# Performance work log

Hardware: AMD Instinct MI355X
Metric: run time of the kernel (lower is better)

Reference implementation:

```python
import jax, jax.numpy as jnp
import numpy as np

B, T, D = 4, 2048, 1024
H, KD, VD = 16, 64, 64  # num_heads, key_dim, value_dim; H*KD == D


def setup_inputs() -> dict:
    key = jax.random.key(0)
    ks = jax.random.split(key, 10)
    s = 0.02
    return {
        "q_in": jax.random.normal(ks[0], (B, T, D), jnp.float32),
        "v_in": jax.random.normal(ks[1], (B, T, D), jnp.float32),
        "Wq": jax.random.normal(ks[2], (D, H * KD), jnp.float32) * s,
        "bq": jnp.zeros((H * KD,), jnp.float32),
        "Wk": jax.random.normal(ks[3], (D, H * KD), jnp.float32) * s,
        "bk": jnp.zeros((H * KD,), jnp.float32),
        "Wv": jax.random.normal(ks[4], (D, H * VD), jnp.float32) * s,
        "bv": jnp.zeros((H * VD,), jnp.float32),
        "Wo": jax.random.normal(ks[5], (H * VD, D), jnp.float32) * s,
        "bo": jnp.zeros((D,), jnp.float32),
    }


def reference(q_in, v_in, Wq, bq, Wk, bk, Wv, bv, Wo, bo):
    # QKV projections (key defaults to value input)
    q = q_in @ Wq + bq                      # [B,T,H*KD]
    k = v_in @ Wk + bk                      # [B,T,H*KD]
    v = v_in @ Wv + bv                      # [B,T,H*VD]
    q = q.reshape(B, T, H, KD)
    k = k.reshape(B, T, H, KD)
    v = v.reshape(B, T, H, VD)
    # scaled dot-product attention, scores materialized as [B,H,Tq,Tv]
    q = q / jnp.sqrt(jnp.asarray(KD, q.dtype))
    scores = jnp.einsum('bqnh,bvnh->bnqv', q, k)
    weights = jax.nn.softmax(scores, axis=-1)
    out = jnp.einsum('bnqv,bvnh->bqnh', weights, v)  # [B,Tq,H,VD]
    out = out.reshape(B, T, H * VD)
    return out @ Wo + bo                    # [B,T,D]
```

## Files before the change

### kernel.cpp

```cpp
#include <hip/hip_runtime.h>

#define BATCH  4
#define T_SEQ  2048
#define NH     16
#define DMODEL 1024
#define HD     64

typedef float    f32x4 __attribute__((ext_vector_type(4)));
typedef _Float16 f16x8 __attribute__((ext_vector_type(8)));
typedef _Float16 f16x4 __attribute__((ext_vector_type(4)));
typedef __fp16   h16x2 __attribute__((ext_vector_type(2)));

#define LOG2E 1.44269504088896f

__device__ __forceinline__ void lds_load16(const void* g, void* l) {
  __builtin_amdgcn_global_load_lds((const __attribute__((address_space(1))) void*)g,
                                   (__attribute__((address_space(3))) void*)l, 16, 0, 0);
}

__device__ __forceinline__ f16x4 pack4_f16(float a, float b, float c, float d) {
  union { h16x2 h[2]; f16x4 f; } u;
  u.h[0] = __builtin_amdgcn_cvt_pkrtz(a, b);
  u.h[1] = __builtin_amdgcn_cvt_pkrtz(c, d);
  return u.f;
}

__global__ __launch_bounds__(256) void cast2_f32_to_f16(
    const float* __restrict__ a, const float* __restrict__ bsrc,
    _Float16* __restrict__ oa, _Float16* __restrict__ ob, int n4) {
  const float* in = blockIdx.y ? bsrc : a;
  _Float16* out = blockIdx.y ? ob : oa;
  int i = blockIdx.x * 256 + threadIdx.x;
  if (i < n4) {
    float4 v = ((const float4*)in)[i];
    f16x4 o = { (_Float16)v.x, (_Float16)v.y, (_Float16)v.z, (_Float16)v.w };
    ((f16x4*)out)[i] = o;
  }
}

__global__ __launch_bounds__(256) void transcast_w4(
    const float* __restrict__ W0, const float* __restrict__ W1,
    const float* __restrict__ W2, const float* __restrict__ W3,
    _Float16* __restrict__ T0, _Float16* __restrict__ T1,
    _Float16* __restrict__ T2, _Float16* __restrict__ T3) {
  const float* W; _Float16* Wt;
  switch (blockIdx.z) {
    case 0: W = W0; Wt = T0; break;
    case 1: W = W1; Wt = T1; break;
    case 2: W = W2; Wt = T2; break;
    default: W = W3; Wt = T3; break;
  }
  __shared__ float L[64][65];
  const int n0 = blockIdx.x * 64, k0 = blockIdx.y * 64;
  const int tx = threadIdx.x & 15, ty = threadIdx.x >> 4;
#pragma unroll
  for (int i = 0; i < 4; ++i) {
    float4 v = *(const float4*)&W[(size_t)(k0 + ty + 16 * i) * DMODEL + n0 + tx * 4];
    L[ty + 16 * i][tx * 4 + 0] = v.x;
    L[ty + 16 * i][tx * 4 + 1] = v.y;
    L[ty + 16 * i][tx * 4 + 2] = v.z;
    L[ty + 16 * i][tx * 4 + 3] = v.w;
  }
  __syncthreads();
#pragma unroll
  for (int i = 0; i < 4; ++i) {
    int n = n0 + ty + 16 * i;
    f16x4 o;
#pragma unroll
    for (int j = 0; j < 4; ++j) o[j] = (_Float16)L[tx * 4 + j][ty + 16 * i];
    *(f16x4*)&Wt[(size_t)n * DMODEL + k0 + tx * 4] = o;
  }
}

__device__ __forceinline__ void gemm_big_body(
    const _Float16* __restrict__ A, const _Float16* __restrict__ Wt,
    const float* __restrict__ bias, void* __restrict__ Cout, float scale,
    int mode, _Float16* As, _Float16* Bs) {
  const int K = DMODEL;
  const int lane = threadIdx.x & 63, wave = threadIdx.x >> 6;
  const int bid = blockIdx.x + blockIdx.y * gridDim.x;
  const int m0 = ((bid & 7) * 4 + ((bid >> 3) & 3)) * 256;
  const int n0 = (bid >> 5) * 128;
  const int wm = (wave & 1) * 8;
  const int wn = (wave >> 1) * 4;
  const int m16 = lane & 15, quad = lane >> 4;

  const _Float16* ap[8]; const _Float16* bp[4];
#pragma unroll
  for (int j = 0; j < 8; ++j) {
    int g = wave * 8 + j;
    ap[j] = A + (size_t)(m0 + (g >> 1) * 16 + m16) * K + (g & 1) * 32 + quad * 8;
  }
#pragma unroll
  for (int j = 0; j < 4; ++j) {
    int g = wave * 4 + j;
    bp[j] = Wt + (size_t)(n0 + (g >> 1) * 16 + m16) * K + (g & 1) * 32 + quad * 8;
  }

  f32x4 acc[8][4] = {};

  for (int k0 = 0; k0 < 1024; k0 += 64) {
    __syncthreads();
#pragma unroll
    for (int j = 0; j < 8; ++j) lds_load16(ap[j] + k0, As + (wave * 8 + j) * 512);
#pragma unroll
    for (int j = 0; j < 4; ++j) lds_load16(bp[j] + k0, Bs + (wave * 4 + j) * 512);
    __syncthreads();
#pragma unroll
    for (int s = 0; s < 2; ++s) {
      f16x8 bf[4];
#pragma unroll
      for (int t = 0; t < 4; ++t)
        bf[t] = *(const f16x8*)(Bs + (((wn + t) * 2 + s) * 64 + lane) * 8);
#pragma unroll
      for (int mi = 0; mi < 8; ++mi) {
        f16x8 af = *(const f16x8*)(As + (((wm + mi) * 2 + s) * 64 + lane) * 8);
#pragma unroll
        for (int ni = 0; ni < 4; ++ni)
          acc[mi][ni] = __builtin_amdgcn_mfma_f32_16x16x32_f16(af, bf[ni], acc[mi][ni], 0, 0, 0);
      }
    }
  }

  if (mode == 2) {
#pragma unroll
    for (int mi = 0; mi < 8; ++mi)
#pragma unroll
      for (int ni = 0; ni < 4; ++ni) {
        int row = m0 + (wm + mi) * 16 + quad * 4;
        int col = n0 + (wn + ni) * 16 + m16;
        int bb = row >> 11, tt = row & (T_SEQ - 1);
        int hh = col >> 6, dd = col & 63;
        float bv = bias[col];
        f16x4 pv = pack4_f16(acc[mi][ni][0] + bv, acc[mi][ni][1] + bv,
                             acc[mi][ni][2] + bv, acc[mi][ni][3] + bv);
        *(f16x4*)&((_Float16*)Cout)[(((size_t)bb * NH + hh) * HD + dd) * T_SEQ + tt] = pv;
      }
  } else {
#pragma unroll
    for (int mi = 0; mi < 8; ++mi)
#pragma unroll
      for (int r = 0; r < 4; ++r) {
        int row = m0 + (wm + mi) * 16 + quad * 4 + r;
#pragma unroll
        for (int ni = 0; ni < 4; ++ni) {
          int col = n0 + (wn + ni) * 16 + m16;
          float v = (acc[mi][ni][r] + bias[col]) * scale;
          ((_Float16*)Cout)[(size_t)row * DMODEL + col] = (_Float16)v;
        }
      }
  }
}

__global__ __launch_bounds__(256, 2) void gemm_qkv(
    const _Float16* __restrict__ Aq, const _Float16* __restrict__ Av,
    const _Float16* __restrict__ Wq, const _Float16* __restrict__ Wk,
    const _Float16* __restrict__ Wv,
    const float* __restrict__ bq, const float* __restrict__ bk,
    const float* __restrict__ bv,
    _Float16* __restrict__ Cq, _Float16* __restrict__ Ck, _Float16* __restrict__ Cv) {
  __shared__ _Float16 As[256 * 64];
  __shared__ _Float16 Bs[128 * 64];
  const _Float16* A; const _Float16* Wt; const float* bias; _Float16* C;
  float scale; int mode;
  if (blockIdx.z == 0)      { A = Aq; Wt = Wq; bias = bq; C = Cq; scale = 0.125f * LOG2E; mode = 0; }
  else if (blockIdx.z == 1) { A = Av; Wt = Wk; bias = bk; C = Ck; scale = 1.f; mode = 0; }
  else                      { A = Av; Wt = Wv; bias = bv; C = Cv; scale = 1.f; mode = 2; }
  gemm_big_body(A, Wt, bias, C, scale, mode, As, Bs);
}

__global__ __launch_bounds__(256, 3) void gemm_out(
    const _Float16* __restrict__ A, const _Float16* __restrict__ Wt,
    const float* __restrict__ bias, float* __restrict__ Cout) {
  __shared__ _Float16 As[128 * 64], Bs[128 * 64];
  const int K = DMODEL;
  const int lane = threadIdx.x & 63, wave = threadIdx.x >> 6;
  const int bid = blockIdx.x + blockIdx.y * gridDim.x;
  const int m0 = ((bid & 7) * 8 + ((bid >> 3) & 7)) * 128;
  const int n0 = (bid >> 6) * 128;
  const int wm = (wave & 1) * 4, wn = (wave >> 1) * 4;
  const int m16 = lane & 15, quad = lane >> 4;

  const _Float16* ap[4]; const _Float16* bp[4];
#pragma unroll
  for (int i = 0; i < 4; ++i) {
    int gi = wave * 4 + i;
    int row = (gi >> 1) * 16 + m16;
    int kof = (gi & 1) * 32 + quad * 8;
    ap[i] = A  + (size_t)(m0 + row) * K + kof;
    bp[i] = Wt + (size_t)(n0 + row) * K + kof;
  }

  f32x4 acc[4][4] = {};

  for (int k0 = 0; k0 < 1024; k0 += 64) {
    __syncthreads();
#pragma unroll
    for (int i = 0; i < 4; ++i) {
      lds_load16(ap[i] + k0, As + (wave * 4 + i) * 512);
      lds_load16(bp[i] + k0, Bs + (wave * 4 + i) * 512);
    }
    __syncthreads();
#pragma unroll
    for (int s = 0; s < 2; ++s) {
      f16x8 af[4], bf[4];
#pragma unroll
      for (int t = 0; t < 4; ++t) {
        af[t] = *(const f16x8*)(As + (((wm + t) * 2 + s) * 64 + lane) * 8);
        bf[t] = *(const f16x8*)(Bs + (((wn + t) * 2 + s) * 64 + lane) * 8);
      }
#pragma unroll
      for (int mi = 0; mi < 4; ++mi)
#pragma unroll
        for (int ni = 0; ni < 4; ++ni)
          acc[mi][ni] = __builtin_amdgcn_mfma_f32_16x16x32_f16(af[mi], bf[ni], acc[mi][ni], 0, 0, 0);
    }
  }

#pragma unroll
  for (int mi = 0; mi < 4; ++mi)
#pragma unroll
    for (int r = 0; r < 4; ++r) {
      int row = m0 + (wm + mi) * 16 + quad * 4 + r;
#pragma unroll
      for (int ni = 0; ni < 4; ++ni) {
        int col = n0 + (wn + ni) * 16 + m16;
        Cout[(size_t)row * DMODEL + col] = acc[mi][ni][r] + bias[col];
      }
    }
}

__global__ __launch_bounds__(256, 2) void attn_mfma(
    const _Float16* __restrict__ Q, const _Float16* __restrict__ Kb,
    const _Float16* __restrict__ Vt, _Float16* __restrict__ O) {
  __shared__ _Float16 Ks[64 * 64], Vs[64 * 64];
  __shared__ _Float16 Ps[4 * 4096];

  const int lane = threadIdx.x & 63, wave = threadIdx.x >> 6;
  const int m16 = lane & 15, quad = lane >> 4;
  const int h = blockIdx.x;
  const int q0 = blockIdx.y * 256;
  const int b = blockIdx.z;
  const int wq = wave * 64;
  const int wbase = wave * 4096;

  f16x8 qf[4][2];
#pragma unroll
  for (int mi = 0; mi < 4; ++mi)
#pragma unroll
    for (int ki = 0; ki < 2; ++ki) {
      int q = q0 + wq + mi * 16 + m16;
      qf[mi][ki] = *(const f16x8*)(Q + (((size_t)b * T_SEQ + q) * NH + h) * HD + ki * 32 + quad * 8);
    }

  const _Float16 *kp[2], *vp[2];
#pragma unroll
  for (int i = 0; i < 2; ++i) {
    int g = wave * 128 + i * 64 + lane;
    int tk = (g >> 7) * 16 + (g & 15);
    int dkof = ((g >> 6) & 1) * 32 + ((g >> 4) & 3) * 8;
    kp[i] = Kb + (((size_t)b * T_SEQ + tk) * NH + h) * HD + dkof;
    int dvof = (g >> 7) * 16 + (g & 15);
    int tv = ((g >> 6) & 1) * 32 + ((g >> 4) & 3) * 8;
    vp[i] = Vt + (((size_t)b * NH + h) * HD + dvof) * T_SEQ + tv;
  }

  int pw[4][4];
#pragma unroll
  for (int mi = 0; mi < 4; ++mi)
#pragma unroll
    for (int nt = 0; nt < 4; ++nt) {
      int kt = nt >> 1;
      int q8 = ((nt & 1) << 1) | (quad >> 1);
      pw[mi][nt] = wbase + ((mi * 2 + kt) * 64 + q8 * 16 + m16) * 8 + (quad & 1) * 4;
    }

  const f16x8 onef = {(_Float16)1, (_Float16)1, (_Float16)1, (_Float16)1,
                      (_Float16)1, (_Float16)1, (_Float16)1, (_Float16)1};

  f32x4 o_acc[4][4] = {};
  f32x4 l_acc[4] = {};

  for (int kv = 0; kv < T_SEQ; kv += 64) {
    __syncthreads();
#pragma unroll
    for (int i = 0; i < 2; ++i) {
      lds_load16(kp[i] + (size_t)kv * (NH * HD), Ks + (wave * 2 + i) * 512);
      lds_load16(vp[i] + kv, Vs + (wave * 2 + i) * 512);
    }
    __syncthreads();

    f32x4 st[4][4] = {};
#pragma unroll
    for (int nt = 0; nt < 4; ++nt)
#pragma unroll
      for (int ki = 0; ki < 2; ++ki) {
        f16x8 kf = *(const f16x8*)(Ks + ((nt * 2 + ki) * 64 + lane) * 8);
#pragma unroll
        for (int mi = 0; mi < 4; ++mi)
          st[mi][nt] = __builtin_amdgcn_mfma_f32_16x16x32_f16(kf, qf[mi][ki], st[mi][nt], 0, 0, 0);
      }

#pragma unroll
    for (int mi = 0; mi < 4; ++mi)
#pragma unroll
      for (int nt = 0; nt < 4; ++nt) {
        f16x4 p = pack4_f16(__builtin_amdgcn_exp2f(st[mi][nt][0]),
                            __builtin_amdgcn_exp2f(st[mi][nt][1]),
                            __builtin_amdgcn_exp2f(st[mi][nt][2]),
                            __builtin_amdgcn_exp2f(st[mi][nt][3]));
        *(f16x4*)(Ps + pw[mi][nt]) = p;
      }

#pragma unroll
    for (int kt = 0; kt < 2; ++kt) {
      f16x8 pf[4];
#pragma unroll
      for (int mi = 0; mi < 4; ++mi) {
        pf[mi] = *(const f16x8*)(Ps + wbase + ((mi * 2 + kt) * 64 + lane) * 8);
        l_acc[mi] = __builtin_amdgcn_mfma_f32_16x16x32_f16(pf[mi], onef, l_acc[mi], 0, 0, 0);
      }
#pragma unroll
      for (int nd = 0; nd < 4; ++nd) {
        f16x8 vf = *(const f16x8*)(Vs + ((nd * 2 + kt) * 64 + lane) * 8);
#pragma unroll
        for (int mi = 0; mi < 4; ++mi)
          o_acc[mi][nd] = __builtin_amdgcn_mfma_f32_16x16x32_f16(pf[mi], vf, o_acc[mi][nd], 0, 0, 0);
      }
    }
  }

#pragma unroll
  for (int mi = 0; mi < 4; ++mi)
#pragma unroll
    for (int r = 0; r < 4; ++r) {
      float inv = 1.f / l_acc[mi][r];
      int q = q0 + wq + mi * 16 + quad * 4 + r;
#pragma unroll
      for (int nd = 0; nd < 4; ++nd) {
        int d = nd * 16 + m16;
        O[(((size_t)b * T_SEQ + q) * NH + h) * HD + d] = (_Float16)(o_acc[mi][nd][r] * inv);
      }
    }
}

extern "C" void kernel_launch(void* const* d_in, const int* in_sizes, int n_in,
                              void* d_out, int out_size, void* d_ws, size_t ws_size,
                              hipStream_t stream) {
  const float* q_in = (const float*)d_in[0];
  const float* v_in = (const float*)d_in[1];
  const float* Wq   = (const float*)d_in[2];
  const float* bq   = (const float*)d_in[3];
  const float* Wk   = (const float*)d_in[4];
  const float* bk   = (const float*)d_in[5];
  const float* Wv   = (const float*)d_in[6];
  const float* bv   = (const float*)d_in[7];
  const float* Wo   = (const float*)d_in[8];
  const float* bo   = (const float*)d_in[9];
  float* out = (float*)d_out;

  const size_t MB = 1u << 20;
  char* ws = (char*)d_ws;
  _Float16* q16  = (_Float16*)(ws);
  _Float16* v16  = (_Float16*)(ws + 16 * MB);
  _Float16* qbuf = (_Float16*)(ws + 32 * MB);
  _Float16* kbuf = (_Float16*)(ws + 48 * MB);
  _Float16* vtb  = (_Float16*)(ws + 64 * MB);
  _Float16* Wqt  = (_Float16*)(ws + 80 * MB);
  _Float16* Wkt  = (_Float16*)(ws + 82 * MB);
  _Float16* Wvt  = (_Float16*)(ws + 84 * MB);
  _Float16* Wot  = (_Float16*)(ws + 86 * MB);

  const int n4 = BATCH * T_SEQ * DMODEL / 4;
  cast2_f32_to_f16<<<dim3(n4 / 256, 2), 256, 0, stream>>>(q_in, v_in, q16, v16, n4);

  transcast_w4<<<dim3(16, 16, 4), 256, 0, stream>>>(Wq, Wk, Wv, Wo, Wqt, Wkt, Wvt, Wot);

  gemm_qkv<<<dim3(8, 32, 3), 256, 0, stream>>>(q16, v16, Wqt, Wkt, Wvt, bq, bk, bv,
                                               qbuf, kbuf, vtb);

  attn_mfma<<<dim3(16, 8, 4), 256, 0, stream>>>(qbuf, kbuf, vtb, qbuf);

  gemm_out<<<dim3(8, 64), 256, 0, stream>>>(qbuf, Wot, bo, out);
}
```

Baseline: 333.6 us.

## Double-buffer LDS in projection GEMMs with 512-thread blocks and shared body

Rewrites the QKV and output projection GEMMs to use double-buffered LDS tiles. The next K-tile is prefetched while MFMAs run on the current one, which leaves one barrier per iteration. Blocks grow to 8 waves, each owning a 64x64 sub-tile, and the output GEMM now uses the same 256x128 tile body as QKV (grid halved). Costs are doubled LDS use (96KB per block), which may limit occupancy, and fewer blocks for the output GEMM.

Result: slower. 345.8 us (+3.6%).

```diff
diff --git a/kernel.cpp b/kernel.cpp
--- a/kernel.cpp
+++ b/kernel.cpp
@@ -72,63 +72,75 @@
   }
 }
 
-__device__ __forceinline__ void gemm_big_body(
+__device__ __forceinline__ void gemm2_body(
     const _Float16* __restrict__ A, const _Float16* __restrict__ Wt,
     const float* __restrict__ bias, void* __restrict__ Cout, float scale,
-    int mode, _Float16* As, _Float16* Bs) {
+    int mode, _Float16* As0, _Float16* As1, _Float16* Bs0, _Float16* Bs1) {
   const int K = DMODEL;
   const int lane = threadIdx.x & 63, wave = threadIdx.x >> 6;
   const int bid = blockIdx.x + blockIdx.y * gridDim.x;
   const int m0 = ((bid & 7) * 4 + ((bid >> 3) & 3)) * 256;
   const int n0 = (bid >> 5) * 128;
-  const int wm = (wave & 1) * 8;
-  const int wn = (wave >> 1) * 4;
+  const int wm4 = (wave & 3) * 4;
+  const int wn4 = (wave >> 2) * 4;
   const int m16 = lane & 15, quad = lane >> 4;
 
-  const _Float16* ap[8]; const _Float16* bp[4];
-#pragma unroll
-  for (int j = 0; j < 8; ++j) {
-    int g = wave * 8 + j;
-    ap[j] = A + (size_t)(m0 + (g >> 1) * 16 + m16) * K + (g & 1) * 32 + quad * 8;
-  }
+  const _Float16* ap[4]; const _Float16* bp[2];
 #pragma unroll
   for (int j = 0; j < 4; ++j) {
     int g = wave * 4 + j;
+    ap[j] = A + (size_t)(m0 + (g >> 1) * 16 + m16) * K + (g & 1) * 32 + quad * 8;
+  }
+#pragma unroll
+  for (int j = 0; j < 2; ++j) {
+    int g = wave * 2 + j;
     bp[j] = Wt + (size_t)(n0 + (g >> 1) * 16 + m16) * K + (g & 1) * 32 + quad * 8;
   }
 
-  f32x4 acc[8][4] = {};
-
-  for (int k0 = 0; k0 < 1024; k0 += 64) {
-    __syncthreads();
-#pragma unroll
-    for (int j = 0; j < 8; ++j) lds_load16(ap[j] + k0, As + (wave * 8 + j) * 512);
-#pragma unroll
-    for (int j = 0; j < 4; ++j) lds_load16(bp[j] + k0, Bs + (wave * 4 + j) * 512);
-    __syncthreads();
+  f32x4 acc[4][4] = {};
+
+  _Float16 *Ac = As0, *An = As1, *Bc = Bs0, *Bn = Bs1;
+
+#pragma unroll
+  for (int j = 0; j < 4; ++j) lds_load16(ap[j], Ac + (wave * 4 + j) * 512);
+#pragma unroll
+  for (int j = 0; j < 2; ++j) lds_load16(bp[j], Bc + (wave * 2 + j) * 512);
+  __syncthreads();
+
+  for (int kt = 0; kt < 16; ++kt) {
+    if (kt < 15) {
+      const int k0 = (kt + 1) * 64;
+#pragma unroll
+      for (int j = 0; j < 4; ++j) lds_load16(ap[j] + k0, An + (wave * 4 + j) * 512);
+#pragma unroll
+      for (int j = 0; j < 2; ++j) lds_load16(bp[j] + k0, Bn + (wave * 2 + j) * 512);
+    }
 #pragma unroll
     for (int s = 0; s < 2; ++s) {
       f16x8 bf[4];
 #pragma unroll
       for (int t = 0; t < 4; ++t)
-        bf[t] = *(const f16x8*)(Bs + (((wn + t) * 2 + s) * 64 + lane) * 8);
-#pragma unroll
-      for (int mi = 0; mi < 8; ++mi) {
-        f16x8 af = *(const f16x8*)(As + (((wm + mi) * 2 + s) * 64 + lane) * 8);
+        bf[t] = *(const f16x8*)(Bc + (((wn4 + t) * 2 + s) * 64 + lane) * 8);
+#pragma unroll
+      for (int mi = 0; mi < 4; ++mi) {
+        f16x8 af = *(const f16x8*)(Ac + (((wm4 + mi) * 2 + s) * 64 + lane) * 8);
 #pragma unroll
         for (int ni = 0; ni < 4; ++ni)
           acc[mi][ni] = __builtin_amdgcn_mfma_f32_16x16x32_f16(af, bf[ni], acc[mi][ni], 0, 0, 0);
       }
     }
+    __syncthreads();
+    _Float16* tA = Ac; Ac = An; An = tA;
+    _Float16* tB = Bc; Bc = Bn; Bn = tB;
   }
 
   if (mode == 2) {
 #pragma unroll
-    for (int mi = 0; mi < 8; ++mi)
+    for (int mi = 0; mi < 4; ++mi)
 #pragma unroll
       for (int ni = 0; ni < 4; ++ni) {
-        int row = m0 + (wm + mi) * 16 + quad * 4;
-        int col = n0 + (wn + ni) * 16 + m16;
+        int row = m0 + (wm4 + mi) * 16 + quad * 4;
+        int col = n0 + (wn4 + ni) * 16 + m16;
         int bb = row >> 11, tt = row & (T_SEQ - 1);
         int hh = col >> 6, dd = col & 63;
         float bv = bias[col];
@@ -136,98 +148,57 @@
                              acc[mi][ni][2] + bv, acc[mi][ni][3] + bv);
         *(f16x4*)&((_Float16*)Cout)[(((size_t)bb * NH + hh) * HD + dd) * T_SEQ + tt] = pv;
       }
-  } else {
-#pragma unroll
-    for (int mi = 0; mi < 8; ++mi)
+  } else if (mode == 0) {
+#pragma unroll
+    for (int mi = 0; mi < 4; ++mi)
 #pragma unroll
       for (int r = 0; r < 4; ++r) {
-        int row = m0 + (wm + mi) * 16 + quad * 4 + r;
+        int row = m0 + (wm4 + mi) * 16 + quad * 4 + r;
 #pragma unroll
         for (int ni = 0; ni < 4; ++ni) {
-          int col = n0 + (wn + ni) * 16 + m16;
+          int col = n0 + (wn4 + ni) * 16 + m16;
           float v = (acc[mi][ni][r] + bias[col]) * scale;
           ((_Float16*)Cout)[(size_t)row * DMODEL + col] = (_Float16)v;
         }
       }
-  }
-}
-
-__global__ __launch_bounds__(256, 2) void gemm_qkv(
+  } else {
+#pragma unroll
+    for (int mi = 0; mi < 4; ++mi)
+#pragma unroll
+      for (int r = 0; r < 4; ++r) {
+        int row = m0 + (wm4 + mi) * 16 + quad * 4 + r;
+#pragma unroll
+        for (int ni = 0; ni < 4; ++ni) {
+          int col = n0 + (wn4 + ni) * 16 + m16;
+          ((float*)Cout)[(size_t)row * DMODEL + col] = acc[mi][ni][r] + bias[col];
+        }
+      }
+  }
+}
+
+__global__ __launch_bounds__(512, 2) void gemm_qkv(
     const _Float16* __restrict__ Aq, const _Float16* __restrict__ Av,
     const _Float16* __restrict__ Wq, const _Float16* __restrict__ Wk,
     const _Float16* __restrict__ Wv,
     const float* __restrict__ bq, const float* __restrict__ bk,
     const float* __restrict__ bv,
     _Float16* __restrict__ Cq, _Float16* __restrict__ Ck, _Float16* __restrict__ Cv) {
-  __shared__ _Float16 As[256 * 64];
-  __shared__ _Float16 Bs[128 * 64];
+  __shared__ _Float16 As[2][256 * 64];
+  __shared__ _Float16 Bs[2][128 * 64];
   const _Float16* A; const _Float16* Wt; const float* bias; _Float16* C;
   float scale; int mode;
   if (blockIdx.z == 0)      { A = Aq; Wt = Wq; bias = bq; C = Cq; scale = 0.125f * LOG2E; mode = 0; }
   else if (blockIdx.z == 1) { A = Av; Wt = Wk; bias = bk; C = Ck; scale = 1.f; mode = 0; }
   else                      { A = Av; Wt = Wv; bias = bv; C = Cv; scale = 1.f; mode = 2; }
-  gemm_big_body(A, Wt, bias, C, scale, mode, As, Bs);
-}
-
-__global__ __launch_bounds__(256, 3) void gemm_out(
+  gemm2_body(A, Wt, bias, C, scale, mode, As[0], As[1], Bs[0], Bs[1]);
+}
+
+__global__ __launch_bounds__(512, 2) void gemm_out(
     const _Float16* __restrict__ A, const _Float16* __restrict__ Wt,
     const float* __restrict__ bias, float* __restrict__ Cout) {
-  __shared__ _Float16 As[128 * 64], Bs[128 * 64];
-  const int K = DMODEL;
-  const int lane = threadIdx.x & 63, wave = threadIdx.x >> 6;
-  const int bid = blockIdx.x + blockIdx.y * gridDim.x;
-  const int m0 = ((bid & 7) * 8 + ((bid >> 3) & 7)) * 128;
-  const int n0 = (bid >> 6) * 128;
-  const int wm = (wave & 1) * 4, wn = (wave >> 1) * 4;
-  const int m16 = lane & 15, quad = lane >> 4;
-
-  const _Float16* ap[4]; const _Float16* bp[4];
-#pragma unroll
-  for (int i = 0; i < 4; ++i) {
-    int gi = wave * 4 + i;
-    int row = (gi >> 1) * 16 + m16;
-    int kof = (gi & 1) * 32 + quad * 8;
-    ap[i] = A  + (size_t)(m0 + row) * K + kof;
-    bp[i] = Wt + (size_t)(n0 + row) * K + kof;
-  }
-
-  f32x4 acc[4][4] = {};
-
-  for (int k0 = 0; k0 < 1024; k0 += 64) {
-    __syncthreads();
-#pragma unroll
-    for (int i = 0; i < 4; ++i) {
-      lds_load16(ap[i] + k0, As + (wave * 4 + i) * 512);
-      lds_load16(bp[i] + k0, Bs + (wave * 4 + i) * 512);
-    }
-    __syncthreads();
-#pragma unroll
-    for (int s = 0; s < 2; ++s) {
-      f16x8 af[4], bf[4];
-#pragma unroll
-      for (int t = 0; t < 4; ++t) {
-        af[t] = *(const f16x8*)(As + (((wm + t) * 2 + s) * 64 + lane) * 8);
-        bf[t] = *(const f16x8*)(Bs + (((wn + t) * 2 + s) * 64 + lane) * 8);
-      }
-#pragma unroll
-      for (int mi = 0; mi < 4; ++mi)
-#pragma unroll
-        for (int ni = 0; ni < 4; ++ni)
-          acc[mi][ni] = __builtin_amdgcn_mfma_f32_16x16x32_f16(af[mi], bf[ni], acc[mi][ni], 0, 0, 0);
-    }
-  }
-
-#pragma unroll
-  for (int mi = 0; mi < 4; ++mi)
-#pragma unroll
-    for (int r = 0; r < 4; ++r) {
-      int row = m0 + (wm + mi) * 16 + quad * 4 + r;
-#pragma unroll
-      for (int ni = 0; ni < 4; ++ni) {
-        int col = n0 + (wn + ni) * 16 + m16;
-        Cout[(size_t)row * DMODEL + col] = acc[mi][ni][r] + bias[col];
-      }
-    }
+  __shared__ _Float16 As[2][256 * 64];
+  __shared__ _Float16 Bs[2][128 * 64];
+  gemm2_body(A, Wt, bias, Cout, 1.f, 3, As[0], As[1], Bs[0], Bs[1]);
 }
 
 __global__ __launch_bounds__(256, 2) void attn_mfma(
@@ -376,10 +347,10 @@
 
   transcast_w4<<<dim3(16, 16, 4), 256, 0, stream>>>(Wq, Wk, Wv, Wo, Wqt, Wkt, Wvt, Wot);
 
-  gemm_qkv<<<dim3(8, 32, 3), 256, 0, stream>>>(q16, v16, Wqt, Wkt, Wvt, bq, bk, bv,
+  gemm_qkv<<<dim3(8, 32, 3), 512, 0, stream>>>(q16, v16, Wqt, Wkt, Wvt, bq, bk, bv,
                                                qbuf, kbuf, vtb);
 
   attn_mfma<<<dim3(16, 8, 4), 256, 0, stream>>>(qbuf, kbuf, vtb, qbuf);
 
-  gemm_out<<<dim3(8, 64), 256, 0, stream>>>(qbuf, Wot, bo, out);
-}
+  gemm_out<<<dim3(8, 32), 512, 0, stream>>>(qbuf, Wot, bo, out);
+}
```
